# Optimization experiments

Measured on AMD Instinct MI355X. Metric: run time of the kernel, lower is better.

Reference implementation:

```python
import jax, jax.numpy as jnp
import numpy as np

# ---- static config (mirrors build() with the chosen init_kwargs) ----
B, H, W, C = 16, 56, 56, 128
KH, KW = 3, 3          # filter_size
SH, SW = 1, 1          # stride
NF = 256               # n_filters
IN_FEAT = C * KH * KW  # 1152
NNZ = int(1 * 0.2 * IN_FEAT * NF)  # multiple * density * n_parameters = 58982


def _make_indices():
    """Replicates the full='output' sparsity-pattern construction from build()."""
    rng = np.random.default_rng(0)
    per_col = NNZ // NF
    remain = NNZ % NF
    remain_cols = set(rng.choice(NF, remain, replace=False).tolist())
    chunks = []
    for col in rng.permutation(NF):
        k = per_col + (1 if int(col) in remain_cols else 0)
        rows = rng.choice(IN_FEAT, k, replace=False)
        chunks.append(np.stack([rows, np.full(k, col, dtype=np.int64)], axis=1))
    return np.concatenate(chunks, axis=0).astype(np.int32)  # (NNZ, 2) [row, col]


def setup_inputs() -> dict:
    key = jax.random.key(0)
    k1, k2 = jax.random.split(key)
    x = jax.random.normal(k1, (B, H, W, C), dtype=jnp.float32)
    limit = float(np.sqrt(6.0 / (IN_FEAT + NF)))  # glorot_uniform on the sparse values
    kernel = jax.random.uniform(k2, (NNZ,), jnp.float32, -limit, limit)
    bias = jnp.zeros((NF,), jnp.float32)
    indices = jnp.asarray(_make_indices())
    return {"x": x, "kernel": kernel, "bias": bias, "indices": indices}


def _im2col_valid(x):
    # tf.image.extract_patches ordering: patch positions row-major (di, dj),
    # channels fastest -> concatenate C-channel slices in (di, dj) order.
    oh = (H - KH) // SH + 1
    ow = (W - KW) // SW + 1
    cols = [x[:, di:di + oh * SH:SH, dj:dj + ow * SW:SW, :]
            for di in range(KH) for dj in range(KW)]
    return jnp.concatenate(cols, axis=-1), oh, ow  # (B, oh, ow, IN_FEAT)


def reference(x, kernel, bias, indices):
    patches, oh, ow = _im2col_valid(x)
    pm = patches.reshape(-1, IN_FEAT)  # (B*oh*ow, IN_FEAT)
    # Sparse (IN_FEAT, NF) weight: scatter values into a dense matrix
    # (indices are unique by construction, so .add == .set and is grad-safe).
    Wm = jnp.zeros((IN_FEAT, NF), dtype=pm.dtype).at[indices[:, 0], indices[:, 1]].add(kernel)
    out = pm @ Wm + bias            # sparse-dense matmul + bias
    out = jax.nn.relu(out)          # activation
    return out.reshape(B, oh, ow, NF)
```

## Files before the change

### kernel.cpp

```cpp
#include <hip/hip_runtime.h>

typedef unsigned short u16;
typedef __bf16 bf16x8 __attribute__((ext_vector_type(8)));
typedef float f32x4 __attribute__((ext_vector_type(4)));

#define B_   16
#define H_   56
#define W_   56
#define C_   128
#define OH_  54
#define OW_  54
#define NF_  256
#define KF_  1152
#define M_   46656
#define NNZ_ 58982

#define XB_ELEMS (B_*H_*W_*C_)
#define WT_ELEMS (36*4*256*8)

__device__ __forceinline__ u16 f2bf(float f) {
    unsigned u = __float_as_uint(f);
    u += 0x7FFFu + ((u >> 16) & 1u);
    return (u16)(u >> 16);
}

__device__ __forceinline__ void gload16(const void* g, void* l) {
    __builtin_amdgcn_global_load_lds(
        (const __attribute__((address_space(1))) unsigned int*)g,
        (__attribute__((address_space(3))) unsigned int*)l,
        16, 0, 0);
}

__global__ __launch_bounds__(256) void cvt_x_kernel(const float* __restrict__ x,
                                                    u16* __restrict__ xb,
                                                    u16* __restrict__ wt) {
    if (blockIdx.x < 144) {
        uint4 z = {0u, 0u, 0u, 0u};
        ((uint4*)wt)[blockIdx.x * 256 + threadIdx.x] = z;
    }
    int i = (blockIdx.x * 256 + threadIdx.x) * 8;
    float4 v0 = *(const float4*)(x + i);
    float4 v1 = *(const float4*)(x + i + 4);
    union { u16 u[8]; uint4 v; } r;
    r.u[0] = f2bf(v0.x); r.u[1] = f2bf(v0.y); r.u[2] = f2bf(v0.z); r.u[3] = f2bf(v0.w);
    r.u[4] = f2bf(v1.x); r.u[5] = f2bf(v1.y); r.u[6] = f2bf(v1.z); r.u[7] = f2bf(v1.w);
    *(uint4*)(xb + i) = r.v;
}

__global__ __launch_bounds__(256) void scatter_kernel(const float* __restrict__ kv,
                                                      const int* __restrict__ idx,
                                                      u16* __restrict__ wt) {
    int t = blockIdx.x * 256 + threadIdx.x;
    if (t >= NNZ_) return;
    int k   = idx[2*t];
    int col = idx[2*t + 1];
    int kt = k >> 5, ks = (k >> 3) & 3, e = k & 7;
    wt[(kt * 4 + ks) * 2048 + col * 8 + e] = f2bf(kv[t]);
}

__global__ __launch_bounds__(256, 3) void spconv_gemm(const u16* __restrict__ xb,
                                                      const u16* __restrict__ wt,
                                                      const float* __restrict__ bias,
                                                      float* __restrict__ out) {
    __shared__ __align__(16) u16 As[3][64 * 32];

    const int t    = threadIdx.x;
    const int lane = t & 63;
    const int wid  = t >> 6;

    const int nwg = gridDim.x;
    const int q = nwg >> 3, r = nwg & 7;
    const int xcd = blockIdx.x & 7, inner = blockIdx.x >> 3;
    const int wg = (xcd < r ? xcd * (q + 1) : r * (q + 1) + (xcd - r) * q) + inner;
    const int m0 = wg * 64;

    const int arow = t >> 2;
    const int kco  = ((t & 3) ^ (arow & 3) ^ ((arow >> 2) & 3)) * 8;
    const u16* a_base;
    {
        int mg  = m0 + arow;
        int bb  = mg / (OH_ * OW_);
        int rem = mg % (OH_ * OW_);
        int ii  = rem / OW_;
        int jj  = rem % OW_;
        a_base = xb + ((bb * H_ + ii) * W_ + jj) * C_;
    }

    const int ks   = lane >> 4;
    const int r16  = lane & 15;
    const int cidx = ks ^ (r16 & 3) ^ ((r16 >> 2) & 3);

    const char* bptr = (const char*)wt + ks * 4096 + (wid * 64 + r16) * 16;

    f32x4 acc[4][4];
    const f32x4 zz = {0.f, 0.f, 0.f, 0.f};
#pragma unroll
    for (int i = 0; i < 4; ++i)
#pragma unroll
        for (int j = 0; j < 4; ++j) acc[i][j] = zz;

    bf16x8 bs[3][4];

#define LOADB(dst, base, imm) \
    asm volatile("global_load_dwordx4 %0, %1, off offset:" imm \
                 : "=v"(dst) : "v"(base))

#define ISSUE_B(si) do {                                                    \
    LOADB(bs[si][0], bptr, "0");   LOADB(bs[si][1], bptr, "256");           \
    LOADB(bs[si][2], bptr, "512"); LOADB(bs[si][3], bptr, "768");           \
    bptr += 16384;                                                          \
} while (0)

#define ISSUE_A(kn, bi) do {                                                \
    int g_  = (kn) >> 2;                                                    \
    int di_ = (g_ * 11) >> 5;                                               \
    int dj_ = g_ - 3 * di_;                                                 \
    int aoff_ = (di_ * W_ + dj_) * C_ + ((kn) & 3) * 32 + kco;              \
    gload16(a_base + aoff_, &As[bi][t * 8]);                                \
} while (0)

#define COMPUTE(bi, si) do {                                                \
    bf16x8 a0_ = *(const bf16x8*)(&As[bi][(r16) * 32 + cidx * 8]);          \
    bf16x8 a1_ = *(const bf16x8*)(&As[bi][(16 + r16) * 32 + cidx * 8]);     \
    bf16x8 a2_ = *(const bf16x8*)(&As[bi][(32 + r16) * 32 + cidx * 8]);     \
    bf16x8 a3_ = *(const bf16x8*)(&As[bi][(48 + r16) * 32 + cidx * 8]);     \
    _Pragma("unroll")                                                       \
    for (int nf = 0; nf < 4; ++nf) {                                        \
        acc[0][nf] = __builtin_amdgcn_mfma_f32_16x16x32_bf16(a0_, bs[si][nf], acc[0][nf], 0, 0, 0); \
        acc[1][nf] = __builtin_amdgcn_mfma_f32_16x16x32_bf16(a1_, bs[si][nf], acc[1][nf], 0, 0, 0); \
        acc[2][nf] = __builtin_amdgcn_mfma_f32_16x16x32_bf16(a2_, bs[si][nf], acc[2][nf], 0, 0, 0); \
        acc[3][nf] = __builtin_amdgcn_mfma_f32_16x16x32_bf16(a3_, bs[si][nf], acc[3][nf], 0, 0, 0); \
    }                                                                       \
} while (0)

#define WAITVM(n) asm volatile("s_waitcnt vmcnt(" #n ")" ::: "memory")
#define BAR() do { __builtin_amdgcn_s_barrier();                            \
                   asm volatile("" ::: "memory"); } while (0)

    ISSUE_B(0);
    ISSUE_A(0, 0);
    ISSUE_B(1);
    ISSUE_A(1, 1);
    ISSUE_A(2, 2);

#pragma unroll
    for (int k = 0; k < 33; ++k) {
        WAITVM(6); BAR();
        ISSUE_B((k + 2) % 3);
        COMPUTE(k % 3, k % 3);
        BAR();
        ISSUE_A(k + 3, k % 3);
    }
    WAITVM(6); BAR();
    ISSUE_B(2);
    COMPUTE(0, 0);
    BAR();
    WAITVM(5); BAR();
    COMPUTE(1, 1);
    WAITVM(0); BAR();
    COMPUTE(2, 2);

#undef LOADB
#undef ISSUE_B
#undef ISSUE_A
#undef COMPUTE
#undef WAITVM
#undef BAR

    const int rgrp = lane >> 4;
#pragma unroll
    for (int nf = 0; nf < 4; ++nf) {
        int col  = wid * 64 + nf * 16 + r16;
        float bv = bias[col];
#pragma unroll
        for (int mf = 0; mf < 4; ++mf) {
#pragma unroll
            for (int rr = 0; rr < 4; ++rr) {
                int row = m0 + mf * 16 + rgrp * 4 + rr;
                float v = acc[mf][nf][rr] + bv;
                out[row * NF_ + col] = fmaxf(v, 0.f);
            }
        }
    }
}

extern "C" void kernel_launch(void* const* d_in, const int* in_sizes, int n_in,
                              void* d_out, int out_size, void* d_ws, size_t ws_size,
                              hipStream_t stream) {
    const float* x    = (const float*)d_in[0];
    const float* kv   = (const float*)d_in[1];
    const float* bias = (const float*)d_in[2];
    const int*   idx  = (const int*)d_in[3];
    float* out = (float*)d_out;

    u16* xb  = (u16*)d_ws;
    u16* wtp = (u16*)((char*)d_ws + (size_t)XB_ELEMS * 2);

    cvt_x_kernel<<<XB_ELEMS / (256 * 8), 256, 0, stream>>>(x, xb, wtp);
    scatter_kernel<<<(NNZ_ + 255) / 256, 256, 0, stream>>>(kv, idx, wtp);
    spconv_gemm<<<M_ / 64, 256, 0, stream>>>(xb, wtp, bias, out);
}
```

Baseline: 42.63 us.

## Give each wave private LDS A-tiles to remove block-wide barriers

Measured after the change: 49.69 us. 16.6% more time.

```diff
diff --git a/kernel.cpp b/kernel.cpp
--- a/kernel.cpp
+++ b/kernel.cpp
@@ -62,7 +62,7 @@
                                                       const u16* __restrict__ wt,
                                                       const float* __restrict__ bias,
                                                       float* __restrict__ out) {
-    __shared__ __align__(16) u16 As[3][64 * 32];
+    __shared__ __align__(16) u16 As[4][3][2048];
 
     const int t    = threadIdx.x;
     const int lane = t & 63;
@@ -74,17 +74,19 @@
     const int wg = (xcd < r ? xcd * (q + 1) : r * (q + 1) + (xcd - r) * q) + inner;
     const int m0 = wg * 64;
 
-    const int arow = t >> 2;
-    const int kco  = ((t & 3) ^ (arow & 3) ^ ((arow >> 2) & 3)) * 8;
-    const u16* a_base;
-    {
-        int mg  = m0 + arow;
+    const int qw  = lane >> 2;
+    const int kco = ((lane & 3) ^ (qw & 3) ^ ((qw >> 2) & 3)) * 8;
+    const u16* a_base[4];
+#pragma unroll
+    for (int c = 0; c < 4; ++c) {
+        int mg  = m0 + c * 16 + qw;
         int bb  = mg / (OH_ * OW_);
         int rem = mg % (OH_ * OW_);
         int ii  = rem / OW_;
         int jj  = rem % OW_;
-        a_base = xb + ((bb * H_ + ii) * W_ + jj) * C_;
-    }
+        a_base[c] = xb + ((bb * H_ + ii) * W_ + jj) * C_;
+    }
+    u16* Asw = &As[wid][0][0];
 
     const int ks   = lane >> 4;
     const int r16  = lane & 15;
@@ -99,15 +101,15 @@
 #pragma unroll
         for (int j = 0; j < 4; ++j) acc[i][j] = zz;
 
-    bf16x8 bs[3][4];
+    bf16x8 bs0[4], bs1[4], bs2[4];
 
 #define LOADB(dst, base, imm) \
     asm volatile("global_load_dwordx4 %0, %1, off offset:" imm \
                  : "=v"(dst) : "v"(base))
 
-#define ISSUE_B(si) do {                                                    \
-    LOADB(bs[si][0], bptr, "0");   LOADB(bs[si][1], bptr, "256");           \
-    LOADB(bs[si][2], bptr, "512"); LOADB(bs[si][3], bptr, "768");           \
+#define ISSUE_B(bset) do {                                                  \
+    LOADB(bset[0], bptr, "0");   LOADB(bset[1], bptr, "256");               \
+    LOADB(bset[2], bptr, "512"); LOADB(bset[3], bptr, "768");               \
     bptr += 16384;                                                          \
 } while (0)
 
@@ -116,56 +118,93 @@
     int di_ = (g_ * 11) >> 5;                                               \
     int dj_ = g_ - 3 * di_;                                                 \
     int aoff_ = (di_ * W_ + dj_) * C_ + ((kn) & 3) * 32 + kco;              \
-    gload16(a_base + aoff_, &As[bi][t * 8]);                                \
+    gload16(a_base[0] + aoff_, Asw + (bi) * 2048);                          \
+    gload16(a_base[1] + aoff_, Asw + (bi) * 2048 + 512);                    \
+    gload16(a_base[2] + aoff_, Asw + (bi) * 2048 + 1024);                   \
+    gload16(a_base[3] + aoff_, Asw + (bi) * 2048 + 1536);                   \
 } while (0)
 
-#define COMPUTE(bi, si) do {                                                \
-    bf16x8 a0_ = *(const bf16x8*)(&As[bi][(r16) * 32 + cidx * 8]);          \
-    bf16x8 a1_ = *(const bf16x8*)(&As[bi][(16 + r16) * 32 + cidx * 8]);     \
-    bf16x8 a2_ = *(const bf16x8*)(&As[bi][(32 + r16) * 32 + cidx * 8]);     \
-    bf16x8 a3_ = *(const bf16x8*)(&As[bi][(48 + r16) * 32 + cidx * 8]);     \
+#define WAITVM(n)  asm volatile("s_waitcnt vmcnt(" #n ")" ::: "memory")
+#define WAITLG0()  asm volatile("s_waitcnt lgkmcnt(0)" ::: "memory")
+#define SB0()      __builtin_amdgcn_sched_barrier(0)
+
+#define PHASE(bi, bset, kn, ISS) do {                                       \
+    WAITVM(16); SB0();                                                      \
+    bf16x8 a0_ = *(const bf16x8*)(Asw + (bi) * 2048 + (r16) * 32 + cidx * 8);        \
+    bf16x8 a1_ = *(const bf16x8*)(Asw + (bi) * 2048 + (16 + r16) * 32 + cidx * 8);   \
+    bf16x8 a2_ = *(const bf16x8*)(Asw + (bi) * 2048 + (32 + r16) * 32 + cidx * 8);   \
+    bf16x8 a3_ = *(const bf16x8*)(Asw + (bi) * 2048 + (48 + r16) * 32 + cidx * 8);   \
+    WAITLG0();                                                              \
+    if (ISS) ISSUE_A(kn, bi);                                               \
+    __builtin_amdgcn_s_setprio(1);                                          \
     _Pragma("unroll")                                                       \
     for (int nf = 0; nf < 4; ++nf) {                                        \
-        acc[0][nf] = __builtin_amdgcn_mfma_f32_16x16x32_bf16(a0_, bs[si][nf], acc[0][nf], 0, 0, 0); \
-        acc[1][nf] = __builtin_amdgcn_mfma_f32_16x16x32_bf16(a1_, bs[si][nf], acc[1][nf], 0, 0, 0); \
-        acc[2][nf] = __builtin_amdgcn_mfma_f32_16x16x32_bf16(a2_, bs[si][nf], acc[2][nf], 0, 0, 0); \
-        acc[3][nf] = __builtin_amdgcn_mfma_f32_16x16x32_bf16(a3_, bs[si][nf], acc[3][nf], 0, 0, 0); \
+        acc[0][nf] = __builtin_amdgcn_mfma_f32_16x16x32_bf16(a0_, bset[nf], acc[0][nf], 0, 0, 0); \
+        acc[1][nf] = __builtin_amdgcn_mfma_f32_16x16x32_bf16(a1_, bset[nf], acc[1][nf], 0, 0, 0); \
+        acc[2][nf] = __builtin_amdgcn_mfma_f32_16x16x32_bf16(a2_, bset[nf], acc[2][nf], 0, 0, 0); \
+        acc[3][nf] = __builtin_amdgcn_mfma_f32_16x16x32_bf16(a3_, bset[nf], acc[3][nf], 0, 0, 0); \
     }                                                                       \
+    __builtin_amdgcn_s_setprio(0);                                          \
+    if (ISS) ISSUE_B(bset);                                                 \
 } while (0)
 
-#define WAITVM(n) asm volatile("s_waitcnt vmcnt(" #n ")" ::: "memory")
-#define BAR() do { __builtin_amdgcn_s_barrier();                            \
-                   asm volatile("" ::: "memory"); } while (0)
-
-    ISSUE_B(0);
-    ISSUE_A(0, 0);
-    ISSUE_B(1);
-    ISSUE_A(1, 1);
-    ISSUE_A(2, 2);
-
-#pragma unroll
-    for (int k = 0; k < 33; ++k) {
-        WAITVM(6); BAR();
-        ISSUE_B((k + 2) % 3);
-        COMPUTE(k % 3, k % 3);
-        BAR();
-        ISSUE_A(k + 3, k % 3);
-    }
-    WAITVM(6); BAR();
-    ISSUE_B(2);
-    COMPUTE(0, 0);
-    BAR();
-    WAITVM(5); BAR();
-    COMPUTE(1, 1);
-    WAITVM(0); BAR();
-    COMPUTE(2, 2);
+    ISSUE_A(0, 0); ISSUE_B(bs0);
+    ISSUE_A(1, 1); ISSUE_B(bs1);
+    ISSUE_A(2, 2); ISSUE_B(bs2);
+
+#pragma unroll
+    for (int k2 = 0; k2 < 11; ++k2) {
+        PHASE(0, bs0, 3 * k2 + 3, 1);
+        PHASE(1, bs1, 3 * k2 + 4, 1);
+        PHASE(2, bs2, 3 * k2 + 5, 1);
+    }
+    { WAITVM(16); SB0();
+      bf16x8 a0_ = *(const bf16x8*)(Asw + 0 * 2048 + (r16) * 32 + cidx * 8);
+      bf16x8 a1_ = *(const bf16x8*)(Asw + 0 * 2048 + (16 + r16) * 32 + cidx * 8);
+      bf16x8 a2_ = *(const bf16x8*)(Asw + 0 * 2048 + (32 + r16) * 32 + cidx * 8);
+      bf16x8 a3_ = *(const bf16x8*)(Asw + 0 * 2048 + (48 + r16) * 32 + cidx * 8);
+#pragma unroll
+      for (int nf = 0; nf < 4; ++nf) {
+        acc[0][nf] = __builtin_amdgcn_mfma_f32_16x16x32_bf16(a0_, bs0[nf], acc[0][nf], 0, 0, 0);
+        acc[1][nf] = __builtin_amdgcn_mfma_f32_16x16x32_bf16(a1_, bs0[nf], acc[1][nf], 0, 0, 0);
+        acc[2][nf] = __builtin_amdgcn_mfma_f32_16x16x32_bf16(a2_, bs0[nf], acc[2][nf], 0, 0, 0);
+        acc[3][nf] = __builtin_amdgcn_mfma_f32_16x16x32_bf16(a3_, bs0[nf], acc[3][nf], 0, 0, 0);
+      }
+    }
+    { WAITVM(8); SB0();
+      bf16x8 a0_ = *(const bf16x8*)(Asw + 1 * 2048 + (r16) * 32 + cidx * 8);
+      bf16x8 a1_ = *(const bf16x8*)(Asw + 1 * 2048 + (16 + r16) * 32 + cidx * 8);
+      bf16x8 a2_ = *(const bf16x8*)(Asw + 1 * 2048 + (32 + r16) * 32 + cidx * 8);
+      bf16x8 a3_ = *(const bf16x8*)(Asw + 1 * 2048 + (48 + r16) * 32 + cidx * 8);
+#pragma unroll
+      for (int nf = 0; nf < 4; ++nf) {
+        acc[0][nf] = __builtin_amdgcn_mfma_f32_16x16x32_bf16(a0_, bs1[nf], acc[0][nf], 0, 0, 0);
+        acc[1][nf] = __builtin_amdgcn_mfma_f32_16x16x32_bf16(a1_, bs1[nf], acc[1][nf], 0, 0, 0);
+        acc[2][nf] = __builtin_amdgcn_mfma_f32_16x16x32_bf16(a2_, bs1[nf], acc[2][nf], 0, 0, 0);
+        acc[3][nf] = __builtin_amdgcn_mfma_f32_16x16x32_bf16(a3_, bs1[nf], acc[3][nf], 0, 0, 0);
+      }
+    }
+    { WAITVM(0); SB0();
+      bf16x8 a0_ = *(const bf16x8*)(Asw + 2 * 2048 + (r16) * 32 + cidx * 8);
+      bf16x8 a1_ = *(const bf16x8*)(Asw + 2 * 2048 + (16 + r16) * 32 + cidx * 8);
+      bf16x8 a2_ = *(const bf16x8*)(Asw + 2 * 2048 + (32 + r16) * 32 + cidx * 8);
+      bf16x8 a3_ = *(const bf16x8*)(Asw + 2 * 2048 + (48 + r16) * 32 + cidx * 8);
+#pragma unroll
+      for (int nf = 0; nf < 4; ++nf) {
+        acc[0][nf] = __builtin_amdgcn_mfma_f32_16x16x32_bf16(a0_, bs2[nf], acc[0][nf], 0, 0, 0);
+        acc[1][nf] = __builtin_amdgcn_mfma_f32_16x16x32_bf16(a1_, bs2[nf], acc[1][nf], 0, 0, 0);
+        acc[2][nf] = __builtin_amdgcn_mfma_f32_16x16x32_bf16(a2_, bs2[nf], acc[2][nf], 0, 0, 0);
+        acc[3][nf] = __builtin_amdgcn_mfma_f32_16x16x32_bf16(a3_, bs2[nf], acc[3][nf], 0, 0, 0);
+      }
+    }
 
 #undef LOADB
 #undef ISSUE_B
 #undef ISSUE_A
-#undef COMPUTE
 #undef WAITVM
-#undef BAR
+#undef WAITLG0
+#undef SB0
+#undef PHASE
 
     const int rgrp = lane >> 4;
 #pragma unroll
```
